# Kernel tuning notes

Measured on AMD Instinct MI355X. Metric: run time of the kernel, lower is better.

Reference implementation:

```python
import jax, jax.numpy as jnp
import numpy as np

N_USERS = 100000
M_ITEMS = 50000
EMBED = 64
N_LAYERS = 3
NNZ = 2400000
BATCH = 8192


def setup_inputs() -> dict:
    key = jax.random.key(0)
    ks = jax.random.split(key, 8)
    user = jax.random.randint(ks[0], (BATCH,), 0, N_USERS)
    item_i = jax.random.randint(ks[1], (BATCH,), 0, M_ITEMS)
    item_j = jax.random.randint(ks[2], (BATCH,), 0, M_ITEMS)
    timestamp = jax.random.uniform(ks[3], (BATCH,), dtype=jnp.float32)
    # symmetric bipartite edge list: user->item and item->user halves
    half = NNZ // 2
    u = jax.random.randint(ks[4], (half,), 0, N_USERS)
    it = jax.random.randint(ks[5], (half,), 0, M_ITEMS) + N_USERS
    edge_src = jnp.concatenate([u, it])
    edge_dst = jnp.concatenate([it, u])
    v = jax.random.uniform(ks[6], (half,), dtype=jnp.float32)
    edge_vals = jnp.concatenate([v, v])  # symmetric normalized weights
    embed_user_0 = jax.random.normal(ks[7], (N_USERS, EMBED), dtype=jnp.float32) * 0.1
    embed_item_0 = jax.random.normal(jax.random.fold_in(key, 99), (M_ITEMS, EMBED), dtype=jnp.float32) * 0.1
    return {
        'user': user, 'item_i': item_i, 'item_j': item_j,
        'timestamp': timestamp, 'split_idx': 0,
        'edge_src': edge_src, 'edge_dst': edge_dst, 'edge_vals': edge_vals,
        'embed_user_0': embed_user_0, 'embed_item_0': embed_item_0,
    }


def reference(user, item_i, item_j, timestamp, split_idx,
              edge_src, edge_dst, edge_vals, embed_user_0, embed_item_0):
    N = N_USERS + M_ITEMS
    # LightGCN propagation: mean over layer-0..n_layers embeddings
    all_emb = jnp.concatenate([embed_user_0, embed_item_0], axis=0)  # [N, D]
    emb = all_emb
    emb_sum = all_emb
    for _ in range(N_LAYERS):
        # sparse.mm(Graph, emb): gather source features along edges, scale, segment-reduce
        emb = jax.ops.segment_sum(edge_vals[:, None] * emb[edge_dst], edge_src,
                                  num_segments=N)
        emb_sum = emb_sum + emb
    light_out = emb_sum / (N_LAYERS + 1)
    embed_user = light_out[:N_USERS]
    embed_item = light_out[N_USERS:]

    ue = embed_user[user]          # [B, D]
    ie = embed_item[item_i]        # [B, D]
    je = embed_item[item_j]        # [B, D]
    prediction_i = jnp.sum(ue * ie, axis=-1)
    prediction_j = jnp.sum(ue * je, axis=-1)

    # reg_loss uses layer-0 embeddings gathered at the batch indices
    u0 = embed_user_0[user]
    i0 = embed_item_0[item_i]
    j0 = embed_item_0[item_j]
    reg_loss = 0.5 * (jnp.sum(u0 * u0) + jnp.sum(i0 * i0) + jnp.sum(j0 * j0)) / user.shape[0]
    return prediction_i, prediction_j, reg_loss
```

## Files before the change

kernel.cpp:

```cpp
#include <hip/hip_runtime.h>
#include <hip/hip_fp16.h>

#define N_USERS 100000
#define M_ITEMS 50000
#define NNODES  (N_USERS + M_ITEMS)
#define EMBED   64
#define BATCH   8192

#define NU_E ((size_t)N_USERS * EMBED)
#define NE   ((size_t)NNODES * EMBED)

#define SBN    512
#define NSB    ((NNODES + SBN - 1) / SBN)
#define CAP    14336
#define CSTR   16
#define PBLK   512
#define PTILE  4688
#define PRED_BLOCKS ((BATCH * 64) / 256)

typedef unsigned int uint;

static __device__ __forceinline__ ushort f2bf(float f) {
    uint u = __float_as_uint(f);
    return (ushort)((u + 0x7fffu + ((u >> 16) & 1u)) >> 16);
}
static __device__ __forceinline__ float bf_lo(uint u) { return __uint_as_float(u << 16); }
static __device__ __forceinline__ float bf_hi(uint u) { return __uint_as_float(u & 0xffff0000u); }
static __device__ __forceinline__ float bfs(ushort u) { return __uint_as_float((uint)u << 16); }

static __device__ __forceinline__ int packe(int d, int fbits) {
    ushort h = __half_as_ushort(__float2half(__int_as_float(fbits)));
    return (int)(((uint)d << 15) | (uint)(h & 0x7fffu));
}
static __device__ __forceinline__ float unp_val(int p) {
    return __half2float(__ushort_as_half((ushort)(p & 0x7fff)));
}

__global__ void init_all(const float* __restrict__ eu, const float* __restrict__ ei,
                         ushort* __restrict__ E0, int* __restrict__ gcur) {
    if (blockIdx.x == 0) {
        for (int i = threadIdx.x; i < NSB; i += 1024) gcur[i * CSTR] = i * CAP;
        return;
    }
    size_t t = (size_t)(blockIdx.x - 1) * 1024 + threadIdx.x;
    const size_t nu4 = NU_E / 4;
    const size_t n4  = NE / 4;
    if (t >= n4) return;
    float4 v = (t < nu4) ? ((const float4*)eu)[t] : ((const float4*)ei)[t - nu4];
    ((ushort4*)E0)[t] = make_ushort4(f2bf(v.x), f2bf(v.y), f2bf(v.z), f2bf(v.w));
}

__global__ void __launch_bounds__(1024)
partition2(const int* __restrict__ src, const int* __restrict__ dst,
           const float* __restrict__ vals, int* __restrict__ gcur,
           int2* __restrict__ ebuf, int nnz) {
    __shared__ int2 data[PTILE];
    __shared__ int  cnt[NSB];
    __shared__ int  cur[NSB];
    __shared__ int  lbeg[NSB];
    __shared__ int  gbase[NSB];
    __shared__ int  wsum[16];
    const int blk = blockIdx.x;
    const int tid = threadIdx.x;
    const int lane = tid & 63, w = tid >> 6;
    const int base = blk * PTILE;
    const int end  = min(base + PTILE, nnz);

    for (int i = tid; i < NSB; i += 1024) cnt[i] = 0;
    __syncthreads();
    for (int i = base + tid; i < end; i += 1024)
        atomicAdd(&cnt[src[i] >> 9], 1);
    __syncthreads();
    int c = (tid < NSB) ? cnt[tid] : 0;
    int v = c;
    #pragma unroll
    for (int off = 1; off < 64; off <<= 1) {
        int t = __shfl_up(v, off);
        if (lane >= off) v += t;
    }
    if (lane == 63) wsum[w] = v;
    __syncthreads();
    int wpre = 0;
    #pragma unroll
    for (int k = 0; k < 16; ++k) wpre += (k < w) ? wsum[k] : 0;
    v += wpre;
    if (tid < NSB) {
        int ex = v - c;
        cur[tid]  = ex;
        lbeg[tid] = ex;
        if (c > 0) gbase[tid] = atomicAdd(&gcur[tid * CSTR], c);
    }
    __syncthreads();
    for (int i = base + tid; i < end; i += 1024) {
        int sv = src[i];
        int d  = dst[i];
        float fv = vals[i];
        if (d >= N_USERS) d -= N_USERS;
        int p = atomicAdd(&cur[sv >> 9], 1);
        data[p] = make_int2((sv & 511) | (d << 9), __float_as_int(fv));
    }
    __syncthreads();
    int grp = tid >> 4, lane16 = tid & 15;
    for (int b = grp; b < NSB; b += 64) {
        int cc = cnt[b];
        if (cc == 0) continue;
        int lb = lbeg[b];
        int gb = gbase[b];
        for (int j = lane16; j < cc; j += 16)
            ebuf[gb + j] = data[lb + j];
    }
}

__global__ void __launch_bounds__(1024)
sb_sort(const int* __restrict__ gcur, const int2* __restrict__ ebuf,
        int2* __restrict__ offs2, int* __restrict__ ep,
        int* __restrict__ perm) {
    __shared__ int cnt[SBN], cur[SBN], bcnt[256];
    __shared__ int wsum[16];
    int sb  = blockIdx.x;
    int tid = threadIdx.x;
    int lane = tid & 63, w = tid >> 6;
    int beg = sb * CAP;
    int end = gcur[sb * CSTR];
    if (tid < SBN) cnt[tid] = 0;
    __syncthreads();
    for (int i = beg + tid; i < end; i += 1024)
        atomicAdd(&cnt[ebuf[i].x & (SBN - 1)], 1);
    __syncthreads();
    int c = (tid < SBN) ? cnt[tid] : 0;
    int v = c;
    #pragma unroll
    for (int off = 1; off < 64; off <<= 1) {
        int t = __shfl_up(v, off);
        if (lane >= off) v += t;
    }
    if (lane == 63) wsum[w] = v;
    __syncthreads();
    if (tid < SBN) {
        int wpre = 0;
        #pragma unroll
        for (int k = 0; k < 8; ++k) wpre += (k < w) ? wsum[k] : 0;
        v += wpre;
        int lbase = v - c;
        int node = sb * SBN + tid;
        if (node < NNODES) offs2[node] = make_int2(beg + lbase, c);
        cur[tid] = lbase;
    }
    __syncthreads();
    for (int i = beg + tid; i < end; i += 1024) {
        int2 e = ebuf[i];
        int p = atomicAdd(&cur[e.x & (SBN - 1)], 1);
        ep[beg + p] = packe(e.x >> 9, e.y);
    }
    __syncthreads();
    if (tid < 256) bcnt[tid] = 0;
    __syncthreads();
    int nodeCount = min(NNODES - sb * SBN, SBN);
    int bin = 0;
    if (tid < nodeCount) {
        bin = 255 - min(cnt[tid], 255);
        atomicAdd(&bcnt[bin], 1);
    }
    __syncthreads();
    int c2 = (tid < 256) ? bcnt[tid] : 0;
    int v2 = c2;
    #pragma unroll
    for (int off = 1; off < 64; off <<= 1) {
        int t = __shfl_up(v2, off);
        if (lane >= off) v2 += t;
    }
    if (tid < 256 && lane == 63) wsum[w] = v2;
    __syncthreads();
    if (tid < 256) {
        int wpre = 0;
        #pragma unroll
        for (int k = 0; k < 4; ++k) wpre += (k < w) ? wsum[k] : 0;
        v2 += wpre;
        cur[tid] = sb * SBN + (v2 - c2);
    }
    __syncthreads();
    if (tid < nodeCount) {
        int rank = atomicAdd(&cur[bin], 1);
        perm[rank] = sb * SBN + tid;
    }
}

__global__ void gather_E(const int2* __restrict__ offs2, const int* __restrict__ ep,
                         const int* __restrict__ perm,
                         const ushort* __restrict__ Eprev, ushort* __restrict__ Enext) {
    int t = blockIdx.x * blockDim.x + threadIdx.x;
    int wave = t >> 6;
    int lane = t & 63;
    int g = lane >> 3;
    int q = lane & 7;
    int ln = wave * 8 + g;
    bool valid = ln < NNODES;
    int node = valid ? perm[ln] : 0;
    int2 od = valid ? offs2[node] : make_int2(0, 0);
    int start = od.x;
    int deg   = od.y;
    const uint4* other = (const uint4*)(Eprev + (node < N_USERS ? NU_E : 0));
    int lastIdx = max(start + deg - 1, 0);

    int md = deg;
    #pragma unroll
    for (int off = 8; off <= 32; off <<= 1) md = max(md, __shfl_xor(md, off));

    float a0=0.f,a1=0.f,a2=0.f,a3=0.f,a4=0.f,a5=0.f,a6=0.f,a7=0.f;
    for (int k = 0; k < md; k += 16) {
        int e[16];
        uint4 r[16];
        #pragma unroll
        for (int c = 0; c < 16; ++c) {
            int idx = (k + c < deg) ? start + k + c : lastIdx;
            e[c] = ep[idx];
            if (k + c >= deg) e[c] = 0;
        }
        #pragma unroll
        for (int c = 0; c < 16; ++c)
            r[c] = other[(size_t)(((uint)e[c]) >> 15) * 8 + q];
        #pragma unroll
        for (int c = 0; c < 16; ++c) {
            float v = unp_val(e[c]);
            a0 = fmaf(v, bf_lo(r[c].x), a0);  a1 = fmaf(v, bf_hi(r[c].x), a1);
            a2 = fmaf(v, bf_lo(r[c].y), a2);  a3 = fmaf(v, bf_hi(r[c].y), a3);
            a4 = fmaf(v, bf_lo(r[c].z), a4);  a5 = fmaf(v, bf_hi(r[c].z), a5);
            a6 = fmaf(v, bf_lo(r[c].w), a6);  a7 = fmaf(v, bf_hi(r[c].w), a7);
        }
    }

    if (!valid) return;
    uint4 o;
    o.x = (uint)f2bf(a0) | ((uint)f2bf(a1) << 16);
    o.y = (uint)f2bf(a2) | ((uint)f2bf(a3) << 16);
    o.z = (uint)f2bf(a4) | ((uint)f2bf(a5) << 16);
    o.w = (uint)f2bf(a6) | ((uint)f2bf(a7) << 16);
    ((uint4*)Enext)[(size_t)node * 8 + q] = o;
}

__global__ void predict_kernel(const int* __restrict__ user, const int* __restrict__ item_i,
                               const int* __restrict__ item_j,
                               const ushort* __restrict__ E0, const ushort* __restrict__ E1,
                               const ushort* __restrict__ E2, const ushort* __restrict__ E3,
                               const float* __restrict__ eu0, const float* __restrict__ ei0,
                               float* __restrict__ out, float* __restrict__ rbuf) {
    __shared__ float rpart[4];
    int t = blockIdx.x * blockDim.x + threadIdx.x;
    int b = t >> 6;
    int d = t & 63;
    int wv = threadIdx.x >> 6;
    float pi = 0.f, pj = 0.f, r = 0.f;
    if (b < BATCH) {
        size_t ru = (size_t)user[b] * EMBED + d;
        size_t ri = ((size_t)N_USERS + item_i[b]) * EMBED + d;
        size_t rj = ((size_t)N_USERS + item_j[b]) * EMBED + d;
        float ue = bfs(E0[ru]) + bfs(E1[ru]) + bfs(E2[ru]) + bfs(E3[ru]);
        float ie = bfs(E0[ri]) + bfs(E1[ri]) + bfs(E2[ri]) + bfs(E3[ri]);
        float je = bfs(E0[rj]) + bfs(E1[rj]) + bfs(E2[rj]) + bfs(E3[rj]);
        pi = ue * ie;
        pj = ue * je;
        float u0 = eu0[(size_t)user[b] * EMBED + d];
        float i0 = ei0[(size_t)item_i[b] * EMBED + d];
        float j0 = ei0[(size_t)item_j[b] * EMBED + d];
        r = u0 * u0 + i0 * i0 + j0 * j0;
    }
    #pragma unroll
    for (int off = 32; off > 0; off >>= 1) {
        pi += __shfl_down(pi, off);
        pj += __shfl_down(pj, off);
        r  += __shfl_down(r,  off);
    }
    if (d == 0 && b < BATCH) {
        out[b]         = pi * (1.0f / 16.0f);
        out[BATCH + b] = pj * (1.0f / 16.0f);
        rpart[wv] = r;
    }
    __syncthreads();
    if (threadIdx.x == 0)
        rbuf[blockIdx.x] = rpart[0] + rpart[1] + rpart[2] + rpart[3];
}

__global__ void finalize_reg(const float* __restrict__ rbuf, float* __restrict__ out) {
    __shared__ float lds[4];
    int tid = threadIdx.x;
    float s = 0.f;
    for (int i = tid; i < PRED_BLOCKS; i += 256) s += rbuf[i];
    #pragma unroll
    for (int off = 32; off > 0; off >>= 1) s += __shfl_down(s, off);
    if ((tid & 63) == 0) lds[tid >> 6] = s;
    __syncthreads();
    if (tid == 0)
        out[2 * BATCH] = (lds[0] + lds[1] + lds[2] + lds[3]) * (0.5f / (float)BATCH);
}

extern "C" void kernel_launch(void* const* d_in, const int* in_sizes, int n_in,
                              void* d_out, int out_size, void* d_ws, size_t ws_size,
                              hipStream_t stream) {
    const int*   user      = (const int*)  d_in[0];
    const int*   item_i    = (const int*)  d_in[1];
    const int*   item_j    = (const int*)  d_in[2];
    const int*   edge_src  = (const int*)  d_in[5];
    const int*   edge_dst  = (const int*)  d_in[6];
    const float* edge_vals = (const float*)d_in[7];
    const float* eu0       = (const float*)d_in[8];
    const float* ei0       = (const float*)d_in[9];
    const int    nnz       = in_sizes[5];

    float* out = (float*)d_out;

    ushort* E0    = (ushort*)d_ws;
    ushort* E1    = E0 + NE;
    ushort* E2    = E1 + NE;
    ushort* E3    = E2 + NE;
    int*    ep    = (int*)(E3 + NE);
    int2*   offs2 = (int2*)(ep + (size_t)NSB * CAP);
    int*    gcur  = (int*)(offs2 + NNODES);
    int*    perm  = gcur + NSB * CSTR;
    float*  rbuf  = (float*)(perm + NNODES);
    int2*   ebuf  = (int2*)E1;

    const int initBlocks = (int)((NE / 4 + 1023) / 1024);

    init_all<<<1 + initBlocks, 1024, 0, stream>>>(eu0, ei0, E0, gcur);
    partition2<<<PBLK, 1024, 0, stream>>>(edge_src, edge_dst, edge_vals,
                                          gcur, ebuf, nnz);
    sb_sort<<<NSB, 1024, 0, stream>>>(gcur, ebuf, offs2, ep, perm);
    const int gblocks = (int)((((NNODES + 7) / 8) * 64 + 255) / 256);
    gather_E<<<gblocks, 256, 0, stream>>>(offs2, ep, perm, E0, E1);
    gather_E<<<gblocks, 256, 0, stream>>>(offs2, ep, perm, E1, E2);
    gather_E<<<gblocks, 256, 0, stream>>>(offs2, ep, perm, E2, E3);
    predict_kernel<<<PRED_BLOCKS, 256, 0, stream>>>(
        user, item_i, item_j, E0, E1, E2, E3, eu0, ei0, out, rbuf);
    finalize_reg<<<1, 256, 0, stream>>>(rbuf, out);
}
```

Measured before the change: 307.8 us.

## Compute last propagation layer only for batch nodes inside fused predict kernel

Removes the third full-graph gather pass and instead computes the layer-3 embedding on the fly only for the user, item_i and item_j rows the batch needs, reading neighbor lists from the sorted edge structure. The prediction kernel also finishes the reg-loss reduction through an atomic accumulator and a last-block ticket, which drops the separate finalize kernel. This avoids propagating about 150K nodes when only about 24K rows are needed. In exchange each batch row walks its neighbor list with scalar ushort loads per lane, and the result now depends on the order of float atomic adds.

```diff
diff --git a/kernel.cpp b/kernel.cpp
--- a/kernel.cpp
+++ b/kernel.cpp
@@ -24,9 +24,9 @@
     uint u = __float_as_uint(f);
     return (ushort)((u + 0x7fffu + ((u >> 16) & 1u)) >> 16);
 }
+static __device__ __forceinline__ float bfs(ushort u) { return __uint_as_float((uint)u << 16); }
 static __device__ __forceinline__ float bf_lo(uint u) { return __uint_as_float(u << 16); }
 static __device__ __forceinline__ float bf_hi(uint u) { return __uint_as_float(u & 0xffff0000u); }
-static __device__ __forceinline__ float bfs(ushort u) { return __uint_as_float((uint)u << 16); }
 
 static __device__ __forceinline__ int packe(int d, int fbits) {
     ushort h = __half_as_ushort(__float2half(__int_as_float(fbits)));
@@ -37,9 +37,11 @@
 }
 
 __global__ void init_all(const float* __restrict__ eu, const float* __restrict__ ei,
-                         ushort* __restrict__ E0, int* __restrict__ gcur) {
+                         ushort* __restrict__ E0, int* __restrict__ gcur,
+                         int* __restrict__ bar, float* __restrict__ facc) {
     if (blockIdx.x == 0) {
         for (int i = threadIdx.x; i < NSB; i += 1024) gcur[i * CSTR] = i * CAP;
+        if (threadIdx.x == 0) { bar[0] = 0; facc[0] = 0.f; }
         return;
     }
     size_t t = (size_t)(blockIdx.x - 1) * 1024 + threadIdx.x;
@@ -238,59 +240,78 @@
     ((uint4*)Enext)[(size_t)node * 8 + q] = o;
 }
 
-__global__ void predict_kernel(const int* __restrict__ user, const int* __restrict__ item_i,
-                               const int* __restrict__ item_j,
-                               const ushort* __restrict__ E0, const ushort* __restrict__ E1,
-                               const ushort* __restrict__ E2, const ushort* __restrict__ E3,
-                               const float* __restrict__ eu0, const float* __restrict__ ei0,
-                               float* __restrict__ out, float* __restrict__ rbuf) {
+static __device__ __forceinline__ float grow(int node, const int2* offs2,
+                                             const int* ep, const ushort* E2, int d) {
+    int2 od = offs2[node];
+    int start = od.x, deg = od.y;
+    const ushort* ob = E2 + (node < N_USERS ? NU_E : 0);
+    float a = 0.f;
+    for (int k = 0; k < deg; k += 8) {
+        int e[8];
+        #pragma unroll
+        for (int c = 0; c < 8; ++c)
+            e[c] = (k + c < deg) ? ep[start + k + c] : 0;
+        #pragma unroll
+        for (int c = 0; c < 8; ++c) {
+            ushort rv = ob[(size_t)(((uint)e[c]) >> 15) * 64 + d];
+            a = fmaf(unp_val(e[c]), bfs(rv), a);
+        }
+    }
+    return a;
+}
+
+__global__ void __launch_bounds__(256)
+predict_fused(const int2* __restrict__ offs2, const int* __restrict__ ep,
+              const ushort* __restrict__ E0, const ushort* __restrict__ E1,
+              const ushort* __restrict__ E2,
+              const int* __restrict__ user, const int* __restrict__ item_i,
+              const int* __restrict__ item_j,
+              const float* __restrict__ eu0, const float* __restrict__ ei0,
+              float* __restrict__ out, int* __restrict__ bar,
+              float* __restrict__ facc) {
     __shared__ float rpart[4];
     int t = blockIdx.x * blockDim.x + threadIdx.x;
     int b = t >> 6;
     int d = t & 63;
     int wv = threadIdx.x >> 6;
-    float pi = 0.f, pj = 0.f, r = 0.f;
-    if (b < BATCH) {
-        size_t ru = (size_t)user[b] * EMBED + d;
-        size_t ri = ((size_t)N_USERS + item_i[b]) * EMBED + d;
-        size_t rj = ((size_t)N_USERS + item_j[b]) * EMBED + d;
-        float ue = bfs(E0[ru]) + bfs(E1[ru]) + bfs(E2[ru]) + bfs(E3[ru]);
-        float ie = bfs(E0[ri]) + bfs(E1[ri]) + bfs(E2[ri]) + bfs(E3[ri]);
-        float je = bfs(E0[rj]) + bfs(E1[rj]) + bfs(E2[rj]) + bfs(E3[rj]);
-        pi = ue * ie;
-        pj = ue * je;
-        float u0 = eu0[(size_t)user[b] * EMBED + d];
-        float i0 = ei0[(size_t)item_i[b] * EMBED + d];
-        float j0 = ei0[(size_t)item_j[b] * EMBED + d];
-        r = u0 * u0 + i0 * i0 + j0 * j0;
-    }
+
+    int u  = user[b];
+    int iv = item_i[b], jv = item_j[b];
+    int ni = N_USERS + iv, nj = N_USERS + jv;
+    float u3 = grow(u,  offs2, ep, E2, d);
+    float i3 = grow(ni, offs2, ep, E2, d);
+    float j3 = grow(nj, offs2, ep, E2, d);
+    size_t ru = (size_t)u  * EMBED + d;
+    size_t ri = (size_t)ni * EMBED + d;
+    size_t rj = (size_t)nj * EMBED + d;
+    float ue = bfs(E0[ru]) + bfs(E1[ru]) + bfs(E2[ru]) + u3;
+    float ie = bfs(E0[ri]) + bfs(E1[ri]) + bfs(E2[ri]) + i3;
+    float je = bfs(E0[rj]) + bfs(E1[rj]) + bfs(E2[rj]) + j3;
+    float pi = ue * ie, pj = ue * je;
+    float u0 = eu0[(size_t)u  * EMBED + d];
+    float i0 = ei0[(size_t)iv * EMBED + d];
+    float j0 = ei0[(size_t)jv * EMBED + d];
+    float r = u0 * u0 + i0 * i0 + j0 * j0;
     #pragma unroll
     for (int off = 32; off > 0; off >>= 1) {
         pi += __shfl_down(pi, off);
         pj += __shfl_down(pj, off);
         r  += __shfl_down(r,  off);
     }
-    if (d == 0 && b < BATCH) {
+    if (d == 0) {
         out[b]         = pi * (1.0f / 16.0f);
         out[BATCH + b] = pj * (1.0f / 16.0f);
         rpart[wv] = r;
     }
     __syncthreads();
-    if (threadIdx.x == 0)
-        rbuf[blockIdx.x] = rpart[0] + rpart[1] + rpart[2] + rpart[3];
-}
-
-__global__ void finalize_reg(const float* __restrict__ rbuf, float* __restrict__ out) {
-    __shared__ float lds[4];
-    int tid = threadIdx.x;
-    float s = 0.f;
-    for (int i = tid; i < PRED_BLOCKS; i += 256) s += rbuf[i];
-    #pragma unroll
-    for (int off = 32; off > 0; off >>= 1) s += __shfl_down(s, off);
-    if ((tid & 63) == 0) lds[tid >> 6] = s;
-    __syncthreads();
-    if (tid == 0)
-        out[2 * BATCH] = (lds[0] + lds[1] + lds[2] + lds[3]) * (0.5f / (float)BATCH);
+    if (threadIdx.x == 0) {
+        float s = rpart[0] + rpart[1] + rpart[2] + rpart[3];
+        __hip_atomic_fetch_add(facc, s, __ATOMIC_RELAXED, __HIP_MEMORY_SCOPE_AGENT);
+        int tk = __hip_atomic_fetch_add(bar, 1, __ATOMIC_ACQ_REL, __HIP_MEMORY_SCOPE_AGENT);
+        if (tk == (int)gridDim.x - 1)
+            out[2 * BATCH] = __hip_atomic_load(facc, __ATOMIC_RELAXED,
+                                               __HIP_MEMORY_SCOPE_AGENT) * (0.5f / (float)BATCH);
+    }
 }
 
 extern "C" void kernel_launch(void* const* d_in, const int* in_sizes, int n_in,
@@ -311,25 +332,23 @@
     ushort* E0    = (ushort*)d_ws;
     ushort* E1    = E0 + NE;
     ushort* E2    = E1 + NE;
-    ushort* E3    = E2 + NE;
-    int*    ep    = (int*)(E3 + NE);
+    int*    ep    = (int*)(E2 + NE);
     int2*   offs2 = (int2*)(ep + (size_t)NSB * CAP);
     int*    gcur  = (int*)(offs2 + NNODES);
     int*    perm  = gcur + NSB * CSTR;
-    float*  rbuf  = (float*)(perm + NNODES);
+    int*    bar   = perm + NNODES;
+    float*  facc  = (float*)(bar + 1);
     int2*   ebuf  = (int2*)E1;
 
     const int initBlocks = (int)((NE / 4 + 1023) / 1024);
 
-    init_all<<<1 + initBlocks, 1024, 0, stream>>>(eu0, ei0, E0, gcur);
+    init_all<<<1 + initBlocks, 1024, 0, stream>>>(eu0, ei0, E0, gcur, bar, facc);
     partition2<<<PBLK, 1024, 0, stream>>>(edge_src, edge_dst, edge_vals,
                                           gcur, ebuf, nnz);
     sb_sort<<<NSB, 1024, 0, stream>>>(gcur, ebuf, offs2, ep, perm);
     const int gblocks = (int)((((NNODES + 7) / 8) * 64 + 255) / 256);
     gather_E<<<gblocks, 256, 0, stream>>>(offs2, ep, perm, E0, E1);
     gather_E<<<gblocks, 256, 0, stream>>>(offs2, ep, perm, E1, E2);
-    gather_E<<<gblocks, 256, 0, stream>>>(offs2, ep, perm, E2, E3);
-    predict_kernel<<<PRED_BLOCKS, 256, 0, stream>>>(
-        user, item_i, item_j, E0, E1, E2, E3, eu0, ei0, out, rbuf);
-    finalize_reg<<<1, 256, 0, stream>>>(rbuf, out);
-}
+    predict_fused<<<PRED_BLOCKS, 256, 0, stream>>>(
+        offs2, ep, E0, E1, E2, user, item_i, item_j, eu0, ei0, out, bar, facc);
+}
```

Measured after the change: 324.1 us. 5.3% more time.
